# Optimization experiments

Measured on AMD Instinct MI355X. Metric: run time of the kernel, lower is better.

## Reference

```python
import jax, jax.numpy as jnp
import numpy as np

BATCH, D_IN, HID, OUT = 16384, 2000, 100, 2
BN_EPS = 1e-5


def _quant_act(x, bit):
    # HAWQ QuantAct: per-tensor symmetric quantization, returns (dequantized x, scale)
    n = 2 ** (bit - 1) - 1
    s = jnp.max(jnp.abs(x)) / n
    q = jnp.clip(jnp.round(x / s), -n - 1, n)
    return q * s, s


def _quant_linear(x, p_sf, W, b, wbit=2, bbit=2):
    # HAWQ QuantLinear: INT-w GEMM with per-tensor weight scale; bias quantized
    # at scale w_s * p_sf; input assumed pre-quantized at scale p_sf.
    nw = 2 ** (wbit - 1) - 1
    w_s = jnp.max(jnp.abs(W)) / nw
    w_int = jnp.clip(jnp.round(W / w_s), -nw - 1, nw)          # INT2 weights in {-2..1}
    b_s = w_s * p_sf
    nb = 2 ** (bbit - 1)
    b_int = jnp.clip(jnp.round(b / b_s), -nb, nb - 1)
    x_int = x / p_sf                                            # integer-valued activations
    return (x_int @ w_int.T + b_int) * b_s


def setup_inputs() -> dict:
    key = jax.random.key(0)
    ks = jax.random.split(key, 5)
    return {
        "sig": jax.random.normal(ks[0], (BATCH, D_IN), dtype=jnp.float32),
        "W1": jax.random.normal(ks[1], (HID, D_IN), dtype=jnp.float32) * 0.02,
        "b1": jax.random.normal(ks[2], (HID,), dtype=jnp.float32) * 0.01,
        "W2": jax.random.normal(ks[3], (OUT, HID), dtype=jnp.float32) * 0.1,
        "b2": jax.random.normal(ks[4], (OUT,), dtype=jnp.float32) * 0.01,
        "gamma": jnp.ones((HID,), dtype=jnp.float32),
        "beta": jnp.zeros((HID,), dtype=jnp.float32),
    }


def reference(sig, W1, b1, W2, b2, gamma, beta):
    x, p_sf = _quant_act(sig, 5)                    # quant_input (5-bit)
    x = jax.nn.relu(_quant_linear(x, p_sf, W1, b1)) # linear1 (2-bit w/b) + relu
    x, p_sf = _quant_act(x, 8)                      # q_relu1 (8-bit)
    # BatchNorm1d(100) in training mode: batch stats, biased variance
    mu = jnp.mean(x, axis=0)
    var = jnp.mean((x - mu) ** 2, axis=0)
    x = (x - mu) * jax.lax.rsqrt(var + BN_EPS) * gamma + beta
    x = jax.nn.relu(_quant_linear(x, p_sf, W2, b2)) # linear2 (2-bit w/b) + relu
    x, p_sf = _quant_act(x, 8)                      # q_relu2 (8-bit)
    return x
```

## Files before the change

### kernel.cpp

```cpp
#include <hip/hip_runtime.h>
#include <hip/hip_bf16.h>
#include <stdint.h>

#define BATCH   16384
#define D_IN    2000
#define HID     100
#define OUT_DIM 2
#define BN_EPS_VAL 1e-5f

#define BK      32
#define BN_PAD  128
#define KT      63
#define W1Q_ELEMS (KT * BN_PAD * BK)

typedef float f32x4 __attribute__((ext_vector_type(4)));
typedef short bf16x8 __attribute__((ext_vector_type(8)));

#define WS_W1Q_OFF 4096
#define WS_H1_OFF  (1u << 20)
#define WS_Q2_OFF  (8u << 20)
#define WS_O2_OFF  (10u << 20)

__device__ __forceinline__ void block_atomic_maxf(float v, float* dst) {
#pragma unroll
    for (int off = 32; off > 0; off >>= 1)
        v = fmaxf(v, __shfl_xor(v, off, 64));
    __shared__ float sm[8];
    const int w = threadIdx.x >> 6;
    if ((threadIdx.x & 63) == 0) sm[w] = v;
    __syncthreads();
    if (threadIdx.x == 0) {
        const int nw = (blockDim.x + 63) >> 6;
        float m = sm[0];
        for (int i = 1; i < nw; ++i) m = fmaxf(m, sm[i]);
        atomicMax((unsigned int*)dst, __float_as_uint(m));
    }
}

__global__ __launch_bounds__(256)
void k_absmax(const float* __restrict__ sig, const float* __restrict__ W1,
              const float* __restrict__ W2, float* __restrict__ F) {
    float m = 0.0f;
    const int b = blockIdx.x;
    if (b < 2048) {
        const float4* p = (const float4*)sig;
        const int n4 = BATCH * D_IN / 4;
        for (int i = b * 256 + threadIdx.x; i < n4; i += 2048 * 256) {
            float4 v = p[i];
            m = fmaxf(m, fmaxf(fmaxf(fabsf(v.x), fabsf(v.y)),
                               fmaxf(fabsf(v.z), fabsf(v.w))));
        }
        block_atomic_maxf(m, &F[0]);
    } else if (b < 2064) {
        const float4* p = (const float4*)W1;
        const int n4 = HID * D_IN / 4;
        for (int i = (b - 2048) * 256 + threadIdx.x; i < n4; i += 16 * 256) {
            float4 v = p[i];
            m = fmaxf(m, fmaxf(fmaxf(fabsf(v.x), fabsf(v.y)),
                               fmaxf(fabsf(v.z), fabsf(v.w))));
        }
        block_atomic_maxf(m, &F[1]);
    } else {
        if (threadIdx.x < OUT_DIM * HID) m = fabsf(W2[threadIdx.x]);
        block_atomic_maxf(m, &F[2]);
    }
}

__global__ __launch_bounds__(256)
void k_prep(const float* __restrict__ W1, const float* __restrict__ b1,
            const float* __restrict__ W2, float* __restrict__ F,
            unsigned short* __restrict__ w1q) {
    const int tid = blockIdx.x * 256 + threadIdx.x;
    const float ws1 = F[1];
    if (tid < W1Q_ELEMS) {
        const int kt = tid >> 12;
        const int r  = tid & 4095;
        const int n  = r >> 5;
        const int kk = r & 31;
        const int k  = kt * 32 + kk;
        float q = 0.0f;
        if (n < HID && k < D_IN) {
            q = rintf(W1[n * D_IN + k] / ws1);
            q = fminf(fmaxf(q, -2.0f), 1.0f);
        }
        w1q[tid] = (unsigned short)(__float_as_uint(q) >> 16);
    } else if (tid < W1Q_ELEMS + HID) {
        const int h = tid - W1Q_ELEMS;
        const float s1 = F[0] / 15.0f;
        const float bs = ws1 * s1;
        F[16 + h] = fminf(fmaxf(rintf(b1[h] / bs), -2.0f), 1.0f);
    } else if (tid < W1Q_ELEMS + HID + OUT_DIM * HID) {
        const int j = tid - (W1Q_ELEMS + HID);
        const float ws2 = F[2];
        F[116 + j] = fminf(fmaxf(rintf(W2[j] / ws2), -2.0f), 1.0f);
    }
}

__global__ __launch_bounds__(256)
void k_gemm1(const float* __restrict__ sig, const unsigned short* __restrict__ w1q,
             float* __restrict__ F, float* __restrict__ h1) {
    __shared__ unsigned short As[32][40];
    __shared__ unsigned short Bs[128][40];
    const int tid  = threadIdx.x;
    const int lane = tid & 63;
    const int wid  = tid >> 6;
    const float s1  = F[0] / 15.0f;
    const float bs1 = F[1] * s1;
    const int m0 = blockIdx.x * 32;

    const int ar  = tid >> 3;
    const int akl = (tid & 7) * 4;
    const float* aptr = sig + (size_t)(m0 + ar) * D_IN + akl;

    const int rh = (wid & 1) * 16;
    const int ng = (wid >> 1) * 4;
    const int fr = lane & 15;
    const int fk = (lane >> 4) * 8;

    f32x4 acc[4] = {};

    for (int kt = 0; kt < KT; ++kt) {
        const int kbase = kt * BK;
        float4 v;
        if (kbase + akl < D_IN) v = *(const float4*)(aptr + kbase);
        else                    v = make_float4(0.f, 0.f, 0.f, 0.f);
        ushort4 qa;
        {
            float q;
            q = fminf(fmaxf(rintf(v.x / s1), -16.f), 15.f); qa.x = (unsigned short)(__float_as_uint(q) >> 16);
            q = fminf(fmaxf(rintf(v.y / s1), -16.f), 15.f); qa.y = (unsigned short)(__float_as_uint(q) >> 16);
            q = fminf(fmaxf(rintf(v.z / s1), -16.f), 15.f); qa.z = (unsigned short)(__float_as_uint(q) >> 16);
            q = fminf(fmaxf(rintf(v.w / s1), -16.f), 15.f); qa.w = (unsigned short)(__float_as_uint(q) >> 16);
        }
        *(ushort4*)&As[ar][akl] = qa;
        {
            const uint4* bt = (const uint4*)(w1q + (size_t)kt * (BN_PAD * BK));
            uint4 b0 = bt[tid];
            uint4 b1v = bt[tid + 256];
            *(uint4*)&Bs[tid >> 2][(tid & 3) * 8] = b0;
            *(uint4*)&Bs[(tid + 256) >> 2][(tid & 3) * 8] = b1v;
        }
        __syncthreads();
        bf16x8 a = *(const bf16x8*)&As[rh + fr][fk];
#pragma unroll
        for (int t = 0; t < 4; ++t) {
            bf16x8 b = *(const bf16x8*)&Bs[(ng + t) * 16 + fr][fk];
            acc[t] = __builtin_amdgcn_mfma_f32_16x16x32_bf16(a, b, acc[t], 0, 0, 0);
        }
        __syncthreads();
    }

    float lmax = 0.0f;
#pragma unroll
    for (int t = 0; t < 4; ++t) {
        const int n = (ng + t) * 16 + fr;
        if (n < HID) {
            const float bi = F[16 + n];
#pragma unroll
            for (int r = 0; r < 4; ++r) {
                const int m = m0 + rh + (lane >> 4) * 4 + r;
                float h = (acc[t][r] + bi) * bs1;
                h = fmaxf(h, 0.0f);
                h1[(size_t)m * HID + n] = h;
                lmax = fmaxf(lmax, h);
            }
        }
    }
    block_atomic_maxf(lmax, &F[3]);
}

__global__ __launch_bounds__(256)
void k_quant_h(const float* __restrict__ h1, unsigned char* __restrict__ q2,
               const float* __restrict__ F, unsigned int* __restrict__ S1,
               unsigned int* __restrict__ S2) {
    __shared__ unsigned int ls1[HID], ls2[HID];
    if (threadIdx.x < HID) { ls1[threadIdx.x] = 0u; ls2[threadIdx.x] = 0u; }
    __syncthreads();
    const float s2 = F[3] / 127.0f;
    const int base = blockIdx.x * 6400;
#pragma unroll 5
    for (int it = 0; it < 25; ++it) {
        const int idx = base + it * 256 + threadIdx.x;
        const float h = h1[idx];
        const int q = (int)fminf(rintf(h / s2), 127.0f);
        q2[idx] = (unsigned char)q;
        const int c = idx % HID;
        atomicAdd(&ls1[c], (unsigned int)q);
        atomicAdd(&ls2[c], (unsigned int)(q * q));
    }
    __syncthreads();
    if (threadIdx.x < HID) {
        atomicAdd(&S1[threadIdx.x], ls1[threadIdx.x]);
        atomicAdd(&S2[threadIdx.x], ls2[threadIdx.x]);
    }
}

__global__ void k_bnprep(const float* __restrict__ b2, float* __restrict__ F,
                         const unsigned int* __restrict__ S1,
                         const unsigned int* __restrict__ S2) {
    const int t = threadIdx.x;
    const float s2  = F[3] / 127.0f;
    const float ws2 = F[2];
    const float bs2 = ws2 * s2;
    if (t < HID) {
        const double sd   = (double)s2;
        const double mean = sd * ((double)S1[t] / 16384.0);
        const double ex2  = sd * sd * ((double)S2[t] / 16384.0);
        const double var  = ex2 - mean * mean;
        const float varf  = (float)var;
        const float vpe   = varf + BN_EPS_VAL;
        const float rf    = (float)(1.0 / sqrt((double)vpe));
        F[320 + t] = (float)mean;
        F[420 + t] = rf;
    }
    if (t < OUT_DIM) F[920 + t] = fminf(fmaxf(rintf(b2[t] / bs2), -2.0f), 1.0f);
    if (t == 64) F[922] = bs2;
}

__global__ __launch_bounds__(256)
void k_gemm2(const unsigned char* __restrict__ q2, float* __restrict__ F,
             const float* __restrict__ gamma, const float* __restrict__ beta,
             float* __restrict__ out2) {
    __shared__ float sw[2 * HID], smu[HID], sr[HID], sg[HID], sb[HID];
    __shared__ float ssc[4];
    const int t = threadIdx.x;
    if (t < 2 * HID) sw[t] = F[116 + t];
    if (t < HID) { smu[t] = F[320 + t]; sr[t] = F[420 + t]; sg[t] = gamma[t]; sb[t] = beta[t]; }
    if (t == 200) ssc[0] = F[3] / 127.0f;
    if (t == 201) ssc[1] = F[922];
    if (t == 202) ssc[2] = F[920];
    if (t == 203) ssc[3] = F[921];
    __syncthreads();
    const int row = blockIdx.x * 256 + t;
    const unsigned int* rp = (const unsigned int*)(q2 + (size_t)row * HID);
    const float s2 = ssc[0];
    float a0 = 0.0f, a1 = 0.0f;
#pragma unroll
    for (int j = 0; j < 25; ++j) {
        const unsigned int u = rp[j];
#pragma unroll
        for (int bb = 0; bb < 4; ++bb) {
            const int h = j * 4 + bb;
            const float q = (float)((u >> (8 * bb)) & 255u);
            const float x2v = q * s2;
            const float xb  = fmaf((x2v - smu[h]) * sr[h], sg[h], sb[h]);
            const float xi  = xb / s2;
            a0 = fmaf(xi, sw[h], a0);
            a1 = fmaf(xi, sw[HID + h], a1);
        }
    }
    const float o0 = fmaxf((a0 + ssc[2]) * ssc[1], 0.0f);
    const float o1 = fmaxf((a1 + ssc[3]) * ssc[1], 0.0f);
    out2[row * 2 + 0] = o0;
    out2[row * 2 + 1] = o1;
    block_atomic_maxf(fmaxf(o0, o1), &F[4]);
}

__global__ __launch_bounds__(256)
void k_final(const float* __restrict__ out2, const float* __restrict__ F,
             float* __restrict__ out) {
    const int i = blockIdx.x * 256 + threadIdx.x;
    const float s3 = F[4] / 127.0f;
    float4 v = ((const float4*)out2)[i];
    float4 r;
    r.x = fminf(fmaxf(rintf(v.x / s3), -128.f), 127.f) * s3;
    r.y = fminf(fmaxf(rintf(v.y / s3), -128.f), 127.f) * s3;
    r.z = fminf(fmaxf(rintf(v.z / s3), -128.f), 127.f) * s3;
    r.w = fminf(fmaxf(rintf(v.w / s3), -128.f), 127.f) * s3;
    ((float4*)out)[i] = r;
}

extern "C" void kernel_launch(void* const* d_in, const int* in_sizes, int n_in,
                              void* d_out, int out_size, void* d_ws, size_t ws_size,
                              hipStream_t stream) {
    const float* sig   = (const float*)d_in[0];
    const float* W1    = (const float*)d_in[1];
    const float* b1    = (const float*)d_in[2];
    const float* W2    = (const float*)d_in[3];
    const float* b2    = (const float*)d_in[4];
    const float* gamma = (const float*)d_in[5];
    const float* beta  = (const float*)d_in[6];

    float* F = (float*)d_ws;
    unsigned short* w1q = (unsigned short*)((char*)d_ws + WS_W1Q_OFF);
    float* h1           = (float*)((char*)d_ws + WS_H1_OFF);
    unsigned char* q2   = (unsigned char*)((char*)d_ws + WS_Q2_OFF);
    float* o2           = (float*)((char*)d_ws + WS_O2_OFF);
    unsigned int* S1    = (unsigned int*)(F + 520);
    unsigned int* S2    = (unsigned int*)(F + 620);

    hipMemsetAsync(d_ws, 0, 4096, stream);
    k_absmax <<<2065, 256, 0, stream>>>(sig, W1, W2, F);
    k_prep   <<<1010, 256, 0, stream>>>(W1, b1, W2, F, w1q);
    k_gemm1  <<<512,  256, 0, stream>>>(sig, w1q, F, h1);
    k_quant_h<<<256,  256, 0, stream>>>(h1, q2, F, S1, S2);
    k_bnprep <<<1,    128, 0, stream>>>(b2, F, S1, S2);
    k_gemm2  <<<64,   256, 0, stream>>>(q2, F, gamma, beta, o2);
    k_final  <<<32,   256, 0, stream>>>(o2, F, (float*)d_out);
}
```

Measured before the change: 294.5 us.

## Restructure gemm1 to register-direct MFMA operands with split-K across waves

gemm1 no longer stages A and B tiles through shared memory with two barriers per K step. Each wave now quantizes its own A fragment in registers and loads B fragments straight from global memory. Waves split the K range in two, one reduction through LDS at the end combines them, and each block covers 64 rows with 8 waves and all 7 N tiles. The launch grids of quant_h (fewer, larger blocks) and gemm2 (more, smaller blocks) are also re-balanced. B fragments are now re-read from global/L2 by every wave, and quant_h runs with far fewer blocks, which could lower its parallelism.

```diff
diff --git a/kernel.cpp b/kernel.cpp
--- a/kernel.cpp
+++ b/kernel.cpp
@@ -96,73 +96,79 @@
     }
 }
 
-__global__ __launch_bounds__(256)
+__global__ __launch_bounds__(512)
 void k_gemm1(const float* __restrict__ sig, const unsigned short* __restrict__ w1q,
              float* __restrict__ F, float* __restrict__ h1) {
-    __shared__ unsigned short As[32][40];
-    __shared__ unsigned short Bs[128][40];
+    __shared__ float red[4][16][113];
     const int tid  = threadIdx.x;
     const int lane = tid & 63;
     const int wid  = tid >> 6;
+    const int rg   = wid & 3;
+    const int ks   = wid >> 2;
     const float s1  = F[0] / 15.0f;
     const float bs1 = F[1] * s1;
-    const int m0 = blockIdx.x * 32;
-
-    const int ar  = tid >> 3;
-    const int akl = (tid & 7) * 4;
-    const float* aptr = sig + (size_t)(m0 + ar) * D_IN + akl;
-
-    const int rh = (wid & 1) * 16;
-    const int ng = (wid >> 1) * 4;
+    const int m0 = blockIdx.x * 64;
+
     const int fr = lane & 15;
-    const int fk = (lane >> 4) * 8;
-
-    f32x4 acc[4] = {};
-
-    for (int kt = 0; kt < KT; ++kt) {
-        const int kbase = kt * BK;
-        float4 v;
-        if (kbase + akl < D_IN) v = *(const float4*)(aptr + kbase);
-        else                    v = make_float4(0.f, 0.f, 0.f, 0.f);
-        ushort4 qa;
+    const int g8 = (lane >> 4) * 8;
+
+    const float* aptr = sig + (size_t)(m0 + rg * 16 + fr) * D_IN;
+
+    f32x4 acc[7] = {};
+
+#pragma unroll 2
+    for (int kt = ks; kt < KT; kt += 2) {
+        const int k0 = kt * BK + g8;
+        float4 va = make_float4(0.f, 0.f, 0.f, 0.f), vb = va;
+        if (k0 < D_IN) {
+            va = *(const float4*)(aptr + k0);
+            vb = *(const float4*)(aptr + k0 + 4);
+        }
+        union { bf16x8 v; unsigned short s[8]; } A;
         {
             float q;
-            q = fminf(fmaxf(rintf(v.x / s1), -16.f), 15.f); qa.x = (unsigned short)(__float_as_uint(q) >> 16);
-            q = fminf(fmaxf(rintf(v.y / s1), -16.f), 15.f); qa.y = (unsigned short)(__float_as_uint(q) >> 16);
-            q = fminf(fmaxf(rintf(v.z / s1), -16.f), 15.f); qa.z = (unsigned short)(__float_as_uint(q) >> 16);
-            q = fminf(fmaxf(rintf(v.w / s1), -16.f), 15.f); qa.w = (unsigned short)(__float_as_uint(q) >> 16);
-        }
-        *(ushort4*)&As[ar][akl] = qa;
-        {
-            const uint4* bt = (const uint4*)(w1q + (size_t)kt * (BN_PAD * BK));
-            uint4 b0 = bt[tid];
-            uint4 b1v = bt[tid + 256];
-            *(uint4*)&Bs[tid >> 2][(tid & 3) * 8] = b0;
-            *(uint4*)&Bs[(tid + 256) >> 2][(tid & 3) * 8] = b1v;
-        }
-        __syncthreads();
-        bf16x8 a = *(const bf16x8*)&As[rh + fr][fk];
-#pragma unroll
-        for (int t = 0; t < 4; ++t) {
-            bf16x8 b = *(const bf16x8*)&Bs[(ng + t) * 16 + fr][fk];
-            acc[t] = __builtin_amdgcn_mfma_f32_16x16x32_bf16(a, b, acc[t], 0, 0, 0);
-        }
-        __syncthreads();
-    }
+            q = fminf(fmaxf(rintf(va.x / s1), -16.f), 15.f); A.s[0] = (unsigned short)(__float_as_uint(q) >> 16);
+            q = fminf(fmaxf(rintf(va.y / s1), -16.f), 15.f); A.s[1] = (unsigned short)(__float_as_uint(q) >> 16);
+            q = fminf(fmaxf(rintf(va.z / s1), -16.f), 15.f); A.s[2] = (unsigned short)(__float_as_uint(q) >> 16);
+            q = fminf(fmaxf(rintf(va.w / s1), -16.f), 15.f); A.s[3] = (unsigned short)(__float_as_uint(q) >> 16);
+            q = fminf(fmaxf(rintf(vb.x / s1), -16.f), 15.f); A.s[4] = (unsigned short)(__float_as_uint(q) >> 16);
+            q = fminf(fmaxf(rintf(vb.y / s1), -16.f), 15.f); A.s[5] = (unsigned short)(__float_as_uint(q) >> 16);
+            q = fminf(fmaxf(rintf(vb.z / s1), -16.f), 15.f); A.s[6] = (unsigned short)(__float_as_uint(q) >> 16);
+            q = fminf(fmaxf(rintf(vb.w / s1), -16.f), 15.f); A.s[7] = (unsigned short)(__float_as_uint(q) >> 16);
+        }
+        const unsigned short* bbase = w1q + ((size_t)kt * BN_PAD + fr) * BK + g8;
+#pragma unroll
+        for (int t = 0; t < 7; ++t) {
+            bf16x8 b = *(const bf16x8*)(bbase + t * 16 * BK);
+            acc[t] = __builtin_amdgcn_mfma_f32_16x16x32_bf16(A.v, b, acc[t], 0, 0, 0);
+        }
+    }
+
+    const int rl = (lane >> 4) * 4;
+    if (ks == 1) {
+#pragma unroll
+        for (int t = 0; t < 7; ++t)
+#pragma unroll
+            for (int r = 0; r < 4; ++r)
+                red[rg][rl + r][t * 16 + fr] = acc[t][r];
+    }
+    __syncthreads();
 
     float lmax = 0.0f;
-#pragma unroll
-    for (int t = 0; t < 4; ++t) {
-        const int n = (ng + t) * 16 + fr;
-        if (n < HID) {
-            const float bi = F[16 + n];
-#pragma unroll
-            for (int r = 0; r < 4; ++r) {
-                const int m = m0 + rh + (lane >> 4) * 4 + r;
-                float h = (acc[t][r] + bi) * bs1;
-                h = fmaxf(h, 0.0f);
-                h1[(size_t)m * HID + n] = h;
-                lmax = fmaxf(lmax, h);
+    if (ks == 0) {
+#pragma unroll
+        for (int t = 0; t < 7; ++t) {
+            const int n = t * 16 + fr;
+            if (n < HID) {
+                const float bi = F[16 + n];
+#pragma unroll
+                for (int r = 0; r < 4; ++r) {
+                    const int m = m0 + rg * 16 + rl + r;
+                    float h = (acc[t][r] + red[rg][rl + r][n] + bi) * bs1;
+                    h = fmaxf(h, 0.0f);
+                    h1[(size_t)m * HID + n] = h;
+                    lmax = fmaxf(lmax, h);
+                }
             }
         }
     }
@@ -177,9 +183,9 @@
     if (threadIdx.x < HID) { ls1[threadIdx.x] = 0u; ls2[threadIdx.x] = 0u; }
     __syncthreads();
     const float s2 = F[3] / 127.0f;
-    const int base = blockIdx.x * 6400;
-#pragma unroll 5
-    for (int it = 0; it < 25; ++it) {
+    const int base = blockIdx.x * 25600;
+#pragma unroll 4
+    for (int it = 0; it < 100; ++it) {
         const int idx = base + it * 256 + threadIdx.x;
         const float h = h1[idx];
         const int q = (int)fminf(rintf(h / s2), 127.0f);
@@ -217,21 +223,23 @@
     if (t == 64) F[922] = bs2;
 }
 
-__global__ __launch_bounds__(256)
+__global__ __launch_bounds__(64)
 void k_gemm2(const unsigned char* __restrict__ q2, float* __restrict__ F,
              const float* __restrict__ gamma, const float* __restrict__ beta,
              float* __restrict__ out2) {
     __shared__ float sw[2 * HID], smu[HID], sr[HID], sg[HID], sb[HID];
     __shared__ float ssc[4];
     const int t = threadIdx.x;
-    if (t < 2 * HID) sw[t] = F[116 + t];
-    if (t < HID) { smu[t] = F[320 + t]; sr[t] = F[420 + t]; sg[t] = gamma[t]; sb[t] = beta[t]; }
-    if (t == 200) ssc[0] = F[3] / 127.0f;
-    if (t == 201) ssc[1] = F[922];
-    if (t == 202) ssc[2] = F[920];
-    if (t == 203) ssc[3] = F[921];
-    __syncthreads();
-    const int row = blockIdx.x * 256 + t;
+    for (int i = t; i < 2 * HID; i += 64) sw[i] = F[116 + i];
+    for (int i = t; i < HID; i += 64) {
+        smu[i] = F[320 + i]; sr[i] = F[420 + i]; sg[i] = gamma[i]; sb[i] = beta[i];
+    }
+    if (t == 60) ssc[0] = F[3] / 127.0f;
+    if (t == 61) ssc[1] = F[922];
+    if (t == 62) ssc[2] = F[920];
+    if (t == 63) ssc[3] = F[921];
+    __syncthreads();
+    const int row = blockIdx.x * 64 + t;
     const unsigned int* rp = (const unsigned int*)(q2 + (size_t)row * HID);
     const float s2 = ssc[0];
     float a0 = 0.0f, a1 = 0.0f;
@@ -292,9 +300,9 @@
     hipMemsetAsync(d_ws, 0, 4096, stream);
     k_absmax <<<2065, 256, 0, stream>>>(sig, W1, W2, F);
     k_prep   <<<1010, 256, 0, stream>>>(W1, b1, W2, F, w1q);
-    k_gemm1  <<<512,  256, 0, stream>>>(sig, w1q, F, h1);
-    k_quant_h<<<256,  256, 0, stream>>>(h1, q2, F, S1, S2);
+    k_gemm1  <<<256,  512, 0, stream>>>(sig, w1q, F, h1);
+    k_quant_h<<<64,   256, 0, stream>>>(h1, q2, F, S1, S2);
     k_bnprep <<<1,    128, 0, stream>>>(b2, F, S1, S2);
-    k_gemm2  <<<64,   256, 0, stream>>>(q2, F, gamma, beta, o2);
+    k_gemm2  <<<256,  64,  0, stream>>>(q2, F, gamma, beta, o2);
     k_final  <<<32,   256, 0, stream>>>(o2, F, (float*)d_out);
 }
```

Measured after the change: 315.9 us. +7.2%, slower.

## Pre-quantize activations into MFMA fragment layout and split-K gemm1 across waves

Applied to the files above, without the earlier changes.

The prep kernel now also quantizes the input signal to bf16 integers and writes it in a per-lane MFMA fragment order to a workspace buffer. gemm1 then loads A and B fragments directly from global memory with no LDS staging or per-iteration barriers. Each of the four waves handles a quarter of K over all 112 padded columns for two row tiles, and the partials are reduced through shared memory. This removes the in-loop quantization and synchronization but adds an extra 64 MB round trip through global memory for the bf16 activations, and loads B without LDS reuse.

```diff
diff --git a/kernel.cpp b/kernel.cpp
--- a/kernel.cpp
+++ b/kernel.cpp
@@ -12,6 +12,7 @@
 #define BN_PAD  128
 #define KT      63
 #define W1Q_ELEMS (KT * BN_PAD * BK)
+#define NPREPA  16128
 
 typedef float f32x4 __attribute__((ext_vector_type(4)));
 typedef short bf16x8 __attribute__((ext_vector_type(8)));
@@ -20,6 +21,11 @@
 #define WS_H1_OFF  (1u << 20)
 #define WS_Q2_OFF  (8u << 20)
 #define WS_O2_OFF  (10u << 20)
+#define WS_QA_OFF  (16u << 20)
+
+__device__ __forceinline__ unsigned short f2bf(float q) {
+    return (unsigned short)(__float_as_uint(q) >> 16);
+}
 
 __device__ __forceinline__ void block_atomic_maxf(float v, float* dst) {
 #pragma unroll
@@ -67,102 +73,125 @@
 }
 
 __global__ __launch_bounds__(256)
-void k_prep(const float* __restrict__ W1, const float* __restrict__ b1,
-            const float* __restrict__ W2, float* __restrict__ F,
-            unsigned short* __restrict__ w1q) {
-    const int tid = blockIdx.x * 256 + threadIdx.x;
-    const float ws1 = F[1];
-    if (tid < W1Q_ELEMS) {
-        const int kt = tid >> 12;
-        const int r  = tid & 4095;
-        const int n  = r >> 5;
-        const int kk = r & 31;
-        const int k  = kt * 32 + kk;
-        float q = 0.0f;
-        if (n < HID && k < D_IN) {
-            q = rintf(W1[n * D_IN + k] / ws1);
-            q = fminf(fmaxf(q, -2.0f), 1.0f);
-        }
-        w1q[tid] = (unsigned short)(__float_as_uint(q) >> 16);
-    } else if (tid < W1Q_ELEMS + HID) {
-        const int h = tid - W1Q_ELEMS;
+void k_prep(const float* __restrict__ sig, const float* __restrict__ W1,
+            const float* __restrict__ b1, const float* __restrict__ W2,
+            float* __restrict__ F, unsigned short* __restrict__ w1q,
+            unsigned short* __restrict__ qa) {
+    const int bid = blockIdx.x;
+    const int t = threadIdx.x;
+    if (bid < NPREPA) {
+        const int c  = bid * 4 + (t >> 6);
+        const int mt = c / KT, kt = c - mt * KT;
+        const int lane = t & 63;
+        const int fr = lane & 15, kg = lane >> 4;
+        const int row = mt * 16 + fr;
+        const int k   = kt * 32 + kg * 8;
         const float s1 = F[0] / 15.0f;
-        const float bs = ws1 * s1;
-        F[16 + h] = fminf(fmaxf(rintf(b1[h] / bs), -2.0f), 1.0f);
-    } else if (tid < W1Q_ELEMS + HID + OUT_DIM * HID) {
-        const int j = tid - (W1Q_ELEMS + HID);
-        const float ws2 = F[2];
-        F[116 + j] = fminf(fmaxf(rintf(W2[j] / ws2), -2.0f), 1.0f);
-    }
-}
-
-__global__ __launch_bounds__(256)
-void k_gemm1(const float* __restrict__ sig, const unsigned short* __restrict__ w1q,
+        float e[8];
+        if (k + 8 <= D_IN) {
+            const float4 va = *(const float4*)(sig + (size_t)row * D_IN + k);
+            const float4 vb = *(const float4*)(sig + (size_t)row * D_IN + k + 4);
+            e[0]=va.x; e[1]=va.y; e[2]=va.z; e[3]=va.w;
+            e[4]=vb.x; e[5]=vb.y; e[6]=vb.z; e[7]=vb.w;
+        } else {
+#pragma unroll
+            for (int j = 0; j < 8; ++j) e[j] = 0.0f;
+        }
+        union { ushort4 u4[2]; unsigned short s[8]; } A;
+#pragma unroll
+        for (int j = 0; j < 8; ++j)
+            A.s[j] = f2bf(fminf(fmaxf(rintf(e[j] / s1), -16.0f), 15.0f));
+        ushort4* dst = (ushort4*)(qa + ((size_t)c * 64 + lane) * 8);
+        dst[0] = A.u4[0];
+        dst[1] = A.u4[1];
+    } else {
+        const int tid = (bid - NPREPA) * 256 + t;
+        const float ws1 = F[1];
+        if (tid < W1Q_ELEMS) {
+            const int kt = tid >> 12;
+            const int r  = tid & 4095;
+            const int n  = r >> 5;
+            const int kk = r & 31;
+            const int k  = kt * 32 + kk;
+            float q = 0.0f;
+            if (n < HID && k < D_IN) {
+                q = rintf(W1[n * D_IN + k] / ws1);
+                q = fminf(fmaxf(q, -2.0f), 1.0f);
+            }
+            w1q[tid] = f2bf(q);
+        } else if (tid < W1Q_ELEMS + HID) {
+            const int h = tid - W1Q_ELEMS;
+            const float bs = ws1 * (F[0] / 15.0f);
+            F[16 + h] = fminf(fmaxf(rintf(b1[h] / bs), -2.0f), 1.0f);
+        } else if (tid < W1Q_ELEMS + HID + OUT_DIM * HID) {
+            const int j = tid - (W1Q_ELEMS + HID);
+            F[116 + j] = fminf(fmaxf(rintf(W2[j] / F[2]), -2.0f), 1.0f);
+        }
+    }
+}
+
+__global__ __launch_bounds__(256)
+void k_gemm1(const unsigned short* __restrict__ qa,
+             const unsigned short* __restrict__ w1q,
              float* __restrict__ F, float* __restrict__ h1) {
-    __shared__ unsigned short As[32][40];
-    __shared__ unsigned short Bs[128][40];
-    const int tid  = threadIdx.x;
-    const int lane = tid & 63;
-    const int wid  = tid >> 6;
-    const float s1  = F[0] / 15.0f;
-    const float bs1 = F[1] * s1;
-    const int m0 = blockIdx.x * 32;
-
-    const int ar  = tid >> 3;
-    const int akl = (tid & 7) * 4;
-    const float* aptr = sig + (size_t)(m0 + ar) * D_IN + akl;
-
-    const int rh = (wid & 1) * 16;
-    const int ng = (wid >> 1) * 4;
-    const int fr = lane & 15;
-    const int fk = (lane >> 4) * 8;
-
-    f32x4 acc[4] = {};
-
-    for (int kt = 0; kt < KT; ++kt) {
-        const int kbase = kt * BK;
-        float4 v;
-        if (kbase + akl < D_IN) v = *(const float4*)(aptr + kbase);
-        else                    v = make_float4(0.f, 0.f, 0.f, 0.f);
-        ushort4 qa;
-        {
-            float q;
-            q = fminf(fmaxf(rintf(v.x / s1), -16.f), 15.f); qa.x = (unsigned short)(__float_as_uint(q) >> 16);
-            q = fminf(fmaxf(rintf(v.y / s1), -16.f), 15.f); qa.y = (unsigned short)(__float_as_uint(q) >> 16);
-            q = fminf(fmaxf(rintf(v.z / s1), -16.f), 15.f); qa.z = (unsigned short)(__float_as_uint(q) >> 16);
-            q = fminf(fmaxf(rintf(v.w / s1), -16.f), 15.f); qa.w = (unsigned short)(__float_as_uint(q) >> 16);
-        }
-        *(ushort4*)&As[ar][akl] = qa;
-        {
-            const uint4* bt = (const uint4*)(w1q + (size_t)kt * (BN_PAD * BK));
-            uint4 b0 = bt[tid];
-            uint4 b1v = bt[tid + 256];
-            *(uint4*)&Bs[tid >> 2][(tid & 3) * 8] = b0;
-            *(uint4*)&Bs[(tid + 256) >> 2][(tid & 3) * 8] = b1v;
-        }
-        __syncthreads();
-        bf16x8 a = *(const bf16x8*)&As[rh + fr][fk];
-#pragma unroll
-        for (int t = 0; t < 4; ++t) {
-            bf16x8 b = *(const bf16x8*)&Bs[(ng + t) * 16 + fr][fk];
-            acc[t] = __builtin_amdgcn_mfma_f32_16x16x32_bf16(a, b, acc[t], 0, 0, 0);
-        }
-        __syncthreads();
-    }
+    __shared__ float red[3][32][113];
+    const int t    = threadIdx.x;
+    const int lane = t & 63;
+    const int ks   = t >> 6;
+    const float bs1 = F[1] * (F[0] / 15.0f);
+    const int mt0 = blockIdx.x * 2;
+    const int fr  = lane & 15;
+    const int g8  = (lane >> 4) * 8;
+
+    const int kt0 = ks * 16;
+    const int kt1 = (ks == 3) ? KT : kt0 + 16;
+
+    f32x4 accA[7] = {}, accB[7] = {};
+
+    for (int kt = kt0; kt < kt1; ++kt) {
+        const bf16x8 a0 = *(const bf16x8*)(qa + (((size_t)mt0 * KT + kt) * 64 + lane) * 8);
+        const bf16x8 a1 = *(const bf16x8*)(qa + (((size_t)(mt0 + 1) * KT + kt) * 64 + lane) * 8);
+        const unsigned short* bbase = w1q + ((size_t)kt * BN_PAD + fr) * BK + g8;
+#pragma unroll
+        for (int tt = 0; tt < 7; ++tt) {
+            const bf16x8 b = *(const bf16x8*)(bbase + tt * 16 * BK);
+            accA[tt] = __builtin_amdgcn_mfma_f32_16x16x32_bf16(a0, b, accA[tt], 0, 0, 0);
+            accB[tt] = __builtin_amdgcn_mfma_f32_16x16x32_bf16(a1, b, accB[tt], 0, 0, 0);
+        }
+    }
+
+    const int rl = (lane >> 4) * 4;
+    if (ks != 0) {
+#pragma unroll
+        for (int tt = 0; tt < 7; ++tt)
+#pragma unroll
+            for (int r = 0; r < 4; ++r) {
+                red[ks - 1][rl + r][tt * 16 + fr]      = accA[tt][r];
+                red[ks - 1][16 + rl + r][tt * 16 + fr] = accB[tt][r];
+            }
+    }
+    __syncthreads();
 
     float lmax = 0.0f;
-#pragma unroll
-    for (int t = 0; t < 4; ++t) {
-        const int n = (ng + t) * 16 + fr;
-        if (n < HID) {
-            const float bi = F[16 + n];
-#pragma unroll
-            for (int r = 0; r < 4; ++r) {
-                const int m = m0 + rh + (lane >> 4) * 4 + r;
-                float h = (acc[t][r] + bi) * bs1;
-                h = fmaxf(h, 0.0f);
-                h1[(size_t)m * HID + n] = h;
-                lmax = fmaxf(lmax, h);
+    if (ks == 0) {
+        const int m0 = blockIdx.x * 32;
+#pragma unroll
+        for (int tt = 0; tt < 7; ++tt) {
+            const int n = tt * 16 + fr;
+            if (n < HID) {
+                const float bi = F[16 + n];
+#pragma unroll
+                for (int r = 0; r < 4; ++r) {
+                    float hA = (accA[tt][r] + red[0][rl + r][n] + red[1][rl + r][n]
+                                + red[2][rl + r][n] + bi) * bs1;
+                    float hB = (accB[tt][r] + red[0][16 + rl + r][n] + red[1][16 + rl + r][n]
+                                + red[2][16 + rl + r][n] + bi) * bs1;
+                    hA = fmaxf(hA, 0.0f);
+                    hB = fmaxf(hB, 0.0f);
+                    h1[(size_t)(m0 + rl + r) * HID + n]      = hA;
+                    h1[(size_t)(m0 + 16 + rl + r) * HID + n] = hB;
+                    lmax = fmaxf(lmax, fmaxf(hA, hB));
+                }
             }
         }
     }
@@ -200,18 +229,15 @@
                          const unsigned int* __restrict__ S2) {
     const int t = threadIdx.x;
     const float s2  = F[3] / 127.0f;
-    const float ws2 = F[2];
-    const float bs2 = ws2 * s2;
+    const float bs2 = F[2] * s2;
     if (t < HID) {
         const double sd   = (double)s2;
         const double mean = sd * ((double)S1[t] / 16384.0);
         const double ex2  = sd * sd * ((double)S2[t] / 16384.0);
         const double var  = ex2 - mean * mean;
-        const float varf  = (float)var;
-        const float vpe   = varf + BN_EPS_VAL;
-        const float rf    = (float)(1.0 / sqrt((double)vpe));
+        const float vpe   = (float)var + BN_EPS_VAL;
         F[320 + t] = (float)mean;
-        F[420 + t] = rf;
+        F[420 + t] = (float)(1.0 / sqrt((double)vpe));
     }
     if (t < OUT_DIM) F[920 + t] = fminf(fmaxf(rintf(b2[t] / bs2), -2.0f), 1.0f);
     if (t == 64) F[922] = bs2;
@@ -286,13 +312,14 @@
     float* h1           = (float*)((char*)d_ws + WS_H1_OFF);
     unsigned char* q2   = (unsigned char*)((char*)d_ws + WS_Q2_OFF);
     float* o2           = (float*)((char*)d_ws + WS_O2_OFF);
+    unsigned short* qa  = (unsigned short*)((char*)d_ws + WS_QA_OFF);
     unsigned int* S1    = (unsigned int*)(F + 520);
     unsigned int* S2    = (unsigned int*)(F + 620);
 
     hipMemsetAsync(d_ws, 0, 4096, stream);
     k_absmax <<<2065, 256, 0, stream>>>(sig, W1, W2, F);
-    k_prep   <<<1010, 256, 0, stream>>>(W1, b1, W2, F, w1q);
-    k_gemm1  <<<512,  256, 0, stream>>>(sig, w1q, F, h1);
+    k_prep   <<<NPREPA + 1010, 256, 0, stream>>>(sig, W1, b1, W2, F, w1q, qa);
+    k_gemm1  <<<512,  256, 0, stream>>>(qa, w1q, F, h1);
     k_quant_h<<<256,  256, 0, stream>>>(h1, q2, F, S1, S2);
     k_bnprep <<<1,    128, 0, stream>>>(b2, F, S1, S2);
     k_gemm2  <<<64,   256, 0, stream>>>(q2, F, gamma, beta, o2);
```

New measurement: 286.9 us. 1.03x faster.
